# Performance work log

Measured on AMD Instinct MI355X. Metric: run time of the kernel, lower is better.

## Reference

```python
import jax, jax.numpy as jnp
import numpy as np

N_EMBD = 1024
QK_DIM = 16


def setup_inputs() -> dict:
    key = jax.random.key(0)
    k1, k2, k3, k4, k5 = jax.random.split(key, 5)
    b, s = 8, 2048
    lim = 1.0 / np.sqrt(N_EMBD)  # torch Linear default init range
    return {
        "x": jax.random.normal(k1, (b, s, N_EMBD), dtype=jnp.float32),
        "w_q": jax.random.uniform(k2, (QK_DIM, N_EMBD), minval=-lim, maxval=lim, dtype=jnp.float32),
        "b_q": jax.random.uniform(k3, (QK_DIM,), minval=-lim, maxval=lim, dtype=jnp.float32),
        "w_k": jax.random.uniform(k4, (QK_DIM, N_EMBD), minval=-lim, maxval=lim, dtype=jnp.float32),
        "b_k": jax.random.uniform(k5, (QK_DIM,), minval=-lim, maxval=lim, dtype=jnp.float32),
    }


def reference(x, w_q, b_q, w_k, b_k):
    # x: [b, s, d_model]
    s = x.shape[-2]
    q = jnp.einsum("bsd,ed->bse", x, w_q) + b_q  # [b, s, qk_dim]
    k = jnp.einsum("bsd,ed->bse", x, w_k) + b_k  # [b, s, qk_dim]
    scale = 1.0 / jnp.sqrt(jnp.asarray(QK_DIM, dtype=x.dtype))
    mask = jnp.arange(s)[:, None] >= jnp.arange(s)[None, :]  # causal [s, s]
    scores = jnp.einsum("bqe,bke->bqk", q, k) * scale  # [b, s, s]
    scores = jnp.where(mask[None], scores, jnp.asarray(-10000.0, dtype=x.dtype))
    probs = jax.nn.softmax(scores, axis=-1)
    return jnp.einsum("bqk,bkv->bqv", probs, x)  # identity OV: weighted sum of x
```

## Files before the change

kernel.cpp:

```cpp
#include <hip/hip_runtime.h>

typedef __attribute__((ext_vector_type(4))) float  f32x4;
typedef __attribute__((ext_vector_type(2))) float  f32x2;
typedef __attribute__((ext_vector_type(8))) short  bf16x8;
typedef __attribute__((ext_vector_type(4))) unsigned int u32x4;

#define MFMA16(a,b,c) __builtin_amdgcn_mfma_f32_16x16x32_bf16(a,b,c,0,0,0)
#define SCL   0.360673760f
#define PBIAS 17.3123405f

static __device__ __forceinline__ unsigned short f2bf(float f){
  unsigned int u = __float_as_uint(f);
  u += 0x7fffu + ((u>>16)&1u);
  return (unsigned short)(u>>16);
}
static __device__ __forceinline__ unsigned int pk2(float a, float b){
  return (unsigned)f2bf(a) | (((unsigned)f2bf(b))<<16);
}
static __device__ __forceinline__ float expfast(float a){
  float e; asm("v_exp_f32 %0, %1" : "=v"(e) : "v"(a)); return e;
}
static __device__ __forceinline__ f32x2 pkfma(f32x2 a, f32x2 b, f32x2 c){
  f32x2 d; asm("v_pk_fma_f32 %0, %1, %2, %3" : "=v"(d) : "v"(a), "v"(b), "v"(c)); return d;
}
static __device__ __forceinline__ f32x2 pkadd(f32x2 a, f32x2 b){
  f32x2 d; asm("v_pk_add_f32 %0, %1, %2" : "=v"(d) : "v"(a), "v"(b)); return d;
}

__global__ __launch_bounds__(256,2) void prep_kernel(
    const float* __restrict__ x,  const float* __restrict__ wq, const float* __restrict__ bq,
    const float* __restrict__ wk, const float* __restrict__ bk,
    unsigned short* __restrict__ qws, unsigned short* __restrict__ kws,
    unsigned char* __restrict__ xpk)
{
  __shared__ __align__(16) unsigned short wlds[32*1032];
  __shared__ __align__(16) unsigned short xlds[64*72];
  const int t  = threadIdx.x;
  const int r0 = blockIdx.x<<6;
  const int b  = r0>>11;
  const int s0 = r0&2047;
  const int l = t&63, w = t>>6, g = l>>4, li = l&15;

  { const int n = t>>3, part = t&7;
    const float* wsrc = (n<16) ? (wq + n*1024) : (wk + (n-16)*1024);
    #pragma unroll
    for(int cc=0; cc<16; ++cc){
      const int d = part*128 + cc*8;
      f32x4 f0 = *(const f32x4*)(wsrc + d);
      f32x4 f1 = *(const f32x4*)(wsrc + d + 4);
      u32x4 p;
      p[0]=pk2(f0[0],f0[1]); p[1]=pk2(f0[2],f0[3]);
      p[2]=pk2(f1[0],f1[1]); p[3]=pk2(f1[2],f1[3]);
      *(u32x4*)(&wlds[n*1032 + d]) = p;
    }
  }
  __syncthreads();

  f32x4 acc0 = {0.f,0.f,0.f,0.f};
  f32x4 acc1 = {0.f,0.f,0.f,0.f};
  const int srow = t>>2, dch = t&3;
  const int dd = t&63, sch = t>>6;

  unsigned char* pdst = xpk + ((size_t)(b*64 + (s0>>5) + (sch>>1)))*65536
                      + (size_t)(dd>>4)*1024 + (size_t)(sch&1)*512 + (size_t)(dd&15)*16;

  for(int it=0; it<16; ++it){
    { const float* xp = x + (size_t)(r0+srow)*1024 + it*64 + dch*16;
      f32x4 a0 = *(const f32x4*)(xp);
      f32x4 a1 = *(const f32x4*)(xp+4);
      f32x4 a2 = *(const f32x4*)(xp+8);
      f32x4 a3 = *(const f32x4*)(xp+12);
      u32x4 p0, p1;
      p0[0]=pk2(a0[0],a0[1]); p0[1]=pk2(a0[2],a0[3]);
      p0[2]=pk2(a1[0],a1[1]); p0[3]=pk2(a1[2],a1[3]);
      p1[0]=pk2(a2[0],a2[1]); p1[1]=pk2(a2[2],a2[3]);
      p1[2]=pk2(a3[0],a3[1]); p1[3]=pk2(a3[2],a3[3]);
      *(u32x4*)(&xlds[srow*72 + dch*16])     = p0;
      *(u32x4*)(&xlds[srow*72 + dch*16 + 8]) = p1;
    }
    __syncthreads();
    #pragma unroll
    for(int ks=0; ks<2; ++ks){
      bf16x8 a  = *(const bf16x8*)(&xlds[(16*w+li)*72       + ks*32 + g*8]);
      bf16x8 b0 = *(const bf16x8*)(&wlds[ li*1032     + it*64 + ks*32 + g*8]);
      bf16x8 b1 = *(const bf16x8*)(&wlds[(16+li)*1032 + it*64 + ks*32 + g*8]);
      acc0 = MFMA16(a,b0,acc0);
      acc1 = MFMA16(a,b1,acc1);
    }
    {
      unsigned short v[16];
      #pragma unroll
      for(int jj=0; jj<16; ++jj) v[jj] = xlds[(sch*16 + jj)*72 + dd];
      u32x4 o0, o1;
      o0[0]=(unsigned)v[0]|((unsigned)v[1]<<16);   o0[1]=(unsigned)v[2]|((unsigned)v[3]<<16);
      o0[2]=(unsigned)v[4]|((unsigned)v[5]<<16);   o0[3]=(unsigned)v[6]|((unsigned)v[7]<<16);
      o1[0]=(unsigned)v[8]|((unsigned)v[9]<<16);   o1[1]=(unsigned)v[10]|((unsigned)v[11]<<16);
      o1[2]=(unsigned)v[12]|((unsigned)v[13]<<16); o1[3]=(unsigned)v[14]|((unsigned)v[15]<<16);
      unsigned char* dst = pdst + (size_t)it*4096;
      *(u32x4*)(dst)       = o0;
      *(u32x4*)(dst + 256) = o1;
    }
    __syncthreads();
  }
  #pragma unroll
  for(int reg=0; reg<4; ++reg){
    const int sr = r0 + 16*w + 4*g + reg;
    qws[(size_t)sr*16 + li] = f2bf(acc0[reg] + bq[li]);
    kws[(size_t)sr*16 + li] = f2bf(acc1[reg] + bk[li]);
  }
}

__global__ __launch_bounds__(256,3) void attn_kernel(
    const unsigned short* __restrict__ qws, const unsigned short* __restrict__ kws,
    const unsigned char* __restrict__ xpk, float* __restrict__ out)
{
  __shared__ __align__(16) unsigned char pshare[16384];
  __shared__ float psL[64];
  const int t = threadIdx.x;
  const int l = t&63, w = t>>6, g = l>>4, li = l&15;
  const int bi = blockIdx.x;
  const int b = bi&7;
  const int j = bi>>3;
  const int qb = 31-(j>>2), dq = j&3;
  const int q0 = qb<<6, d0 = dq<<8, nt = qb + 1;

  const int kperm = ((li>>2)<<3) + (li&3);

  const bf16x8 zero8 = {0,0,0,0,0,0,0,0};
  bf16x8 qfr = zero8;
  if(g < 2) qfr = *(const bf16x8*)(qws + ((size_t)(b*2048 + q0 + 16*w + li)<<4) + 8*g);
  const int qg = q0 + 16*w + li;

  f32x4 acc[4][4];
  #pragma unroll
  for(int i=0;i<4;++i)
    #pragma unroll
    for(int jj=0;jj<4;++jj){ acc[i][jj][0]=0.f; acc[i][jj][1]=0.f; acc[i][jj][2]=0.f; acc[i][jj][3]=0.f; }
  f32x2 spv = {0.f, 0.f};

  const unsigned char* xq = xpk + (size_t)(b*64)*65536 + (size_t)(16*dq + 4*w)*1024 + l*16;
  const unsigned short* kp0 = kws + ((size_t)(b*2048 + kperm)<<4) + 8*g;

  bf16x8 k1 = *(const bf16x8*)(kp0);
  bf16x8 k2 = *(const bf16x8*)(kp0 + 64);
  bf16x8 k3 = *(const bf16x8*)(kp0 + 512);
  bf16x8 k4 = *(const bf16x8*)(kp0 + 576);

  const f32x2 vscl = {SCL, SCL}, vbias = {-PBIAS, -PBIAS};

  int buf = 0;
  for(int tt=0; tt<nt; ++tt){
    const int kv0 = tt<<6;
    u32x4 xc[4], xd[4];
    const unsigned char* xqt = xq + (size_t)(tt*2)*65536;
    #pragma unroll
    for(int df=0; df<4; ++df){
      xc[df] = *(const u32x4*)(xqt + df*1024);
      xd[df] = *(const u32x4*)(xqt + 65536 + df*1024);
    }
    f32x4 z = {0.f,0.f,0.f,0.f};
    f32x4 s1 = MFMA16(k1, qfr, z);
    f32x4 s2 = MFMA16(k2, qfr, z);
    f32x4 s3 = MFMA16(k3, qfr, z);
    f32x4 s4 = MFMA16(k4, qfr, z);
    const int tn = (tt+1 < nt) ? tt+1 : tt;
    const unsigned short* kpn = kp0 + (size_t)(tn<<6)*16;
    bf16x8 n1 = *(const bf16x8*)(kpn);
    bf16x8 n2 = *(const bf16x8*)(kpn + 64);
    bf16x8 n3 = *(const bf16x8*)(kpn + 512);
    bf16x8 n4 = *(const bf16x8*)(kpn + 576);
    f32x2 e[8];
    if(tt < nt-1){
      f32x2 tv[8];
      tv[0] = pkfma((f32x2){s1[0], s1[1]}, vscl, vbias);
      tv[1] = pkfma((f32x2){s1[2], s1[3]}, vscl, vbias);
      tv[2] = pkfma((f32x2){s2[0], s2[1]}, vscl, vbias);
      tv[3] = pkfma((f32x2){s2[2], s2[3]}, vscl, vbias);
      tv[4] = pkfma((f32x2){s3[0], s3[1]}, vscl, vbias);
      tv[5] = pkfma((f32x2){s3[2], s3[3]}, vscl, vbias);
      tv[6] = pkfma((f32x2){s4[0], s4[1]}, vscl, vbias);
      tv[7] = pkfma((f32x2){s4[2], s4[3]}, vscl, vbias);
      #pragma unroll
      for(int i=0;i<8;++i){ e[i][0] = expfast(tv[i][0]); e[i][1] = expfast(tv[i][1]); }
    } else {
      const int b1 = kv0 + 8*g, b2 = kv0 + 32 + 8*g;
      float p[16];
      #pragma unroll
      for(int r=0;r<4;++r){
        p[r]    = (b1+r   <= qg) ? expfast(fmaf(s1[r], SCL, -PBIAS)) : 0.f;
        p[4+r]  = (b1+4+r <= qg) ? expfast(fmaf(s2[r], SCL, -PBIAS)) : 0.f;
        p[8+r]  = (b2+r   <= qg) ? expfast(fmaf(s3[r], SCL, -PBIAS)) : 0.f;
        p[12+r] = (b2+4+r <= qg) ? expfast(fmaf(s4[r], SCL, -PBIAS)) : 0.f;
      }
      #pragma unroll
      for(int i=0;i<8;++i){ e[i][0] = p[2*i]; e[i][1] = p[2*i+1]; }
    }
    {
      f32x2 a0 = pkadd(e[0], e[1]);
      f32x2 a1 = pkadd(e[2], e[3]);
      f32x2 a2 = pkadd(e[4], e[5]);
      f32x2 a3 = pkadd(e[6], e[7]);
      spv = pkadd(spv, pkadd(pkadd(a0,a1), pkadd(a2,a3)));
    }
    { u32x4 avA, avB;
      asm("v_cvt_pk_bf16_f32 %0, %1, %2" : "=v"(avA[0]) : "v"(e[0][0]), "v"(e[0][1]));
      asm("v_cvt_pk_bf16_f32 %0, %1, %2" : "=v"(avA[1]) : "v"(e[1][0]), "v"(e[1][1]));
      asm("v_cvt_pk_bf16_f32 %0, %1, %2" : "=v"(avA[2]) : "v"(e[2][0]), "v"(e[2][1]));
      asm("v_cvt_pk_bf16_f32 %0, %1, %2" : "=v"(avA[3]) : "v"(e[3][0]), "v"(e[3][1]));
      asm("v_cvt_pk_bf16_f32 %0, %1, %2" : "=v"(avB[0]) : "v"(e[4][0]), "v"(e[4][1]));
      asm("v_cvt_pk_bf16_f32 %0, %1, %2" : "=v"(avB[1]) : "v"(e[5][0]), "v"(e[5][1]));
      asm("v_cvt_pk_bf16_f32 %0, %1, %2" : "=v"(avB[2]) : "v"(e[6][0]), "v"(e[6][1]));
      asm("v_cvt_pk_bf16_f32 %0, %1, %2" : "=v"(avB[3]) : "v"(e[7][0]), "v"(e[7][1]));
      *(u32x4*)(&pshare[buf*8192 + w*2048 +        l*16]) = avA;
      *(u32x4*)(&pshare[buf*8192 + w*2048 + 1024 + l*16]) = avB;
    }
    asm volatile("s_waitcnt lgkmcnt(0)" ::: "memory");
    __builtin_amdgcn_sched_barrier(0);
    __builtin_amdgcn_s_barrier();
    __builtin_amdgcn_sched_barrier(0);
    __builtin_amdgcn_s_setprio(1);
    #pragma unroll
    for(int qf=0; qf<4; ++qf){
      bf16x8 aA = *(const bf16x8*)(&pshare[buf*8192 + qf*2048 +        l*16]);
      bf16x8 aB = *(const bf16x8*)(&pshare[buf*8192 + qf*2048 + 1024 + l*16]);
      #pragma unroll
      for(int df=0; df<4; ++df){
        acc[qf][df] = MFMA16(aA, *(const bf16x8*)(&xc[df]), acc[qf][df]);
        acc[qf][df] = MFMA16(aB, *(const bf16x8*)(&xd[df]), acc[qf][df]);
      }
    }
    __builtin_amdgcn_s_setprio(0);
    buf ^= 1; k1=n1; k2=n2; k3=n3; k4=n4;
  }

  float r_ = spv[0] + spv[1];
  r_ += __shfl_xor(r_, 16);
  r_ += __shfl_xor(r_, 32);
  if(l < 16) psL[16*w + l] = r_;
  __syncthreads();
  #pragma unroll
  for(int qf=0; qf<4; ++qf){
    const f32x4 pv = *(const f32x4*)(&psL[16*qf + 4*g]);
    #pragma unroll
    for(int reg=0; reg<4; ++reg){
      const float inv = 1.0f/pv[reg];
      float* op = out + (size_t)(b*2048 + q0 + 16*qf + 4*g + reg)*1024 + d0 + 64*w + li;
      #pragma unroll
      for(int df=0; df<4; ++df) op[df*16] = acc[qf][df][reg]*inv;
    }
  }
}

extern "C" void kernel_launch(void* const* d_in, const int* in_sizes, int n_in,
                              void* d_out, int out_size, void* d_ws, size_t ws_size,
                              hipStream_t stream) {
  (void)in_sizes; (void)n_in; (void)out_size; (void)ws_size;
  const float* x  = (const float*)d_in[0];
  const float* wq = (const float*)d_in[1];
  const float* bq = (const float*)d_in[2];
  const float* wk = (const float*)d_in[3];
  const float* bk = (const float*)d_in[4];
  float* out = (float*)d_out;
  char* ws = (char*)d_ws;
  unsigned short* qws = (unsigned short*)(ws);
  unsigned short* kws = (unsigned short*)(ws + (512<<10));
  unsigned char*  xpk = (unsigned char*)(ws + (2<<20));
  hipLaunchKernelGGL(prep_kernel, dim3(256), dim3(256), 0, stream, x, wq, bq, wk, bk, qws, kws, xpk);
  hipLaunchKernelGGL(attn_kernel, dim3(1024), dim3(256), 0, stream, qws, kws, xpk, out);
}
```

Baseline: 68.65 us.

## Raise attention occupancy to 4 waves and drop K prefetch registers

Raises launch bounds from 3 to 4 blocks per CU and removes the software prefetch of next-tile K fragments, loading K at the top of each iteration instead. The masked last tile now computes all exps once and zeroes masked lanes, so there is a single code path. The aim is to cut VGPR pressure enough for higher occupancy, which would hide latency through more resident waves. The cost is that K load latency is exposed before the score MFMAs, and the tighter register budget could cause spills.

```diff
diff --git a/kernel.cpp b/kernel.cpp
--- a/kernel.cpp
+++ b/kernel.cpp
@@ -110,7 +110,7 @@
   }
 }
 
-__global__ __launch_bounds__(256,3) void attn_kernel(
+__global__ __launch_bounds__(256,4) void attn_kernel(
     const unsigned short* __restrict__ qws, const unsigned short* __restrict__ kws,
     const unsigned char* __restrict__ xpk, float* __restrict__ out)
 {
@@ -141,59 +141,58 @@
   const unsigned char* xq = xpk + (size_t)(b*64)*65536 + (size_t)(16*dq + 4*w)*1024 + l*16;
   const unsigned short* kp0 = kws + ((size_t)(b*2048 + kperm)<<4) + 8*g;
 
-  bf16x8 k1 = *(const bf16x8*)(kp0);
-  bf16x8 k2 = *(const bf16x8*)(kp0 + 64);
-  bf16x8 k3 = *(const bf16x8*)(kp0 + 512);
-  bf16x8 k4 = *(const bf16x8*)(kp0 + 576);
-
   const f32x2 vscl = {SCL, SCL}, vbias = {-PBIAS, -PBIAS};
 
   int buf = 0;
   for(int tt=0; tt<nt; ++tt){
     const int kv0 = tt<<6;
-    u32x4 xc[4], xd[4];
-    const unsigned char* xqt = xq + (size_t)(tt*2)*65536;
-    #pragma unroll
-    for(int df=0; df<4; ++df){
-      xc[df] = *(const u32x4*)(xqt + df*1024);
-      xd[df] = *(const u32x4*)(xqt + 65536 + df*1024);
-    }
+    const unsigned short* kpt = kp0 + (size_t)kv0*16;
+    bf16x8 k1 = *(const bf16x8*)(kpt);
+    bf16x8 k2 = *(const bf16x8*)(kpt + 64);
+    bf16x8 k3 = *(const bf16x8*)(kpt + 512);
+    bf16x8 k4 = *(const bf16x8*)(kpt + 576);
     f32x4 z = {0.f,0.f,0.f,0.f};
     f32x4 s1 = MFMA16(k1, qfr, z);
     f32x4 s2 = MFMA16(k2, qfr, z);
     f32x4 s3 = MFMA16(k3, qfr, z);
     f32x4 s4 = MFMA16(k4, qfr, z);
-    const int tn = (tt+1 < nt) ? tt+1 : tt;
-    const unsigned short* kpn = kp0 + (size_t)(tn<<6)*16;
-    bf16x8 n1 = *(const bf16x8*)(kpn);
-    bf16x8 n2 = *(const bf16x8*)(kpn + 64);
-    bf16x8 n3 = *(const bf16x8*)(kpn + 512);
-    bf16x8 n4 = *(const bf16x8*)(kpn + 576);
+    u32x4 xc[4], xd[4];
+    const unsigned char* xqt = xq + (size_t)(tt*2)*65536;
+    #pragma unroll
+    for(int df=0; df<4; ++df){
+      xc[df] = *(const u32x4*)(xqt + df*1024);
+      xd[df] = *(const u32x4*)(xqt + 65536 + df*1024);
+    }
     f32x2 e[8];
-    if(tt < nt-1){
-      f32x2 tv[8];
-      tv[0] = pkfma((f32x2){s1[0], s1[1]}, vscl, vbias);
-      tv[1] = pkfma((f32x2){s1[2], s1[3]}, vscl, vbias);
-      tv[2] = pkfma((f32x2){s2[0], s2[1]}, vscl, vbias);
-      tv[3] = pkfma((f32x2){s2[2], s2[3]}, vscl, vbias);
-      tv[4] = pkfma((f32x2){s3[0], s3[1]}, vscl, vbias);
-      tv[5] = pkfma((f32x2){s3[2], s3[3]}, vscl, vbias);
-      tv[6] = pkfma((f32x2){s4[0], s4[1]}, vscl, vbias);
-      tv[7] = pkfma((f32x2){s4[2], s4[3]}, vscl, vbias);
-      #pragma unroll
-      for(int i=0;i<8;++i){ e[i][0] = expfast(tv[i][0]); e[i][1] = expfast(tv[i][1]); }
-    } else {
+    {
+      f32x2 tv0 = pkfma((f32x2){s1[0], s1[1]}, vscl, vbias);
+      f32x2 tv1 = pkfma((f32x2){s1[2], s1[3]}, vscl, vbias);
+      f32x2 tv2 = pkfma((f32x2){s2[0], s2[1]}, vscl, vbias);
+      f32x2 tv3 = pkfma((f32x2){s2[2], s2[3]}, vscl, vbias);
+      f32x2 tv4 = pkfma((f32x2){s3[0], s3[1]}, vscl, vbias);
+      f32x2 tv5 = pkfma((f32x2){s3[2], s3[3]}, vscl, vbias);
+      f32x2 tv6 = pkfma((f32x2){s4[0], s4[1]}, vscl, vbias);
+      f32x2 tv7 = pkfma((f32x2){s4[2], s4[3]}, vscl, vbias);
+      e[0][0]=expfast(tv0[0]); e[0][1]=expfast(tv0[1]);
+      e[1][0]=expfast(tv1[0]); e[1][1]=expfast(tv1[1]);
+      e[2][0]=expfast(tv2[0]); e[2][1]=expfast(tv2[1]);
+      e[3][0]=expfast(tv3[0]); e[3][1]=expfast(tv3[1]);
+      e[4][0]=expfast(tv4[0]); e[4][1]=expfast(tv4[1]);
+      e[5][0]=expfast(tv5[0]); e[5][1]=expfast(tv5[1]);
+      e[6][0]=expfast(tv6[0]); e[6][1]=expfast(tv6[1]);
+      e[7][0]=expfast(tv7[0]); e[7][1]=expfast(tv7[1]);
+    }
+    if(tt == nt-1){
       const int b1 = kv0 + 8*g, b2 = kv0 + 32 + 8*g;
-      float p[16];
-      #pragma unroll
-      for(int r=0;r<4;++r){
-        p[r]    = (b1+r   <= qg) ? expfast(fmaf(s1[r], SCL, -PBIAS)) : 0.f;
-        p[4+r]  = (b1+4+r <= qg) ? expfast(fmaf(s2[r], SCL, -PBIAS)) : 0.f;
-        p[8+r]  = (b2+r   <= qg) ? expfast(fmaf(s3[r], SCL, -PBIAS)) : 0.f;
-        p[12+r] = (b2+4+r <= qg) ? expfast(fmaf(s4[r], SCL, -PBIAS)) : 0.f;
+      #pragma unroll
+      for(int i=0;i<4;++i){
+        const int k0 = b1 + 2*i;
+        e[i][0]   = (k0   <= qg) ? e[i][0]   : 0.f;
+        e[i][1]   = (k0+1 <= qg) ? e[i][1]   : 0.f;
+        const int k1_ = b2 + 2*i;
+        e[4+i][0] = (k1_   <= qg) ? e[4+i][0] : 0.f;
+        e[4+i][1] = (k1_+1 <= qg) ? e[4+i][1] : 0.f;
       }
-      #pragma unroll
-      for(int i=0;i<8;++i){ e[i][0] = p[2*i]; e[i][1] = p[2*i+1]; }
     }
     {
       f32x2 a0 = pkadd(e[0], e[1]);
@@ -230,7 +229,7 @@
       }
     }
     __builtin_amdgcn_s_setprio(0);
-    buf ^= 1; k1=n1; k2=n2; k3=n3; k4=n4;
+    buf ^= 1;
   }
 
   float r_ = spv[0] + spv[1];
```

Result: slower. 104.1 us (+51.7%).
